# Performance work log

Measured on AMD Instinct MI355X. Metric: run time of the kernel, lower is better.

The kernel has to match this reference:

```python
import jax, jax.numpy as jnp
import numpy as np

NH = 1024
VS = 50257
CUT0 = 1675          # round(VS/30)
CUT1 = 3 * CUT0      # 5025
N_CLUSTERS = 2
HEAD_SIZE = CUT0 + N_CLUSTERS          # 1677
D0, D1 = NH // 4, NH // 16             # 256, 64
SZ0, SZ1 = CUT1 - CUT0, VS - CUT1      # 3350, 45232


def setup_inputs() -> dict:
    key = jax.random.key(0)
    ks = jax.random.split(key, 8)
    s = 0.02
    return {
        "x": jax.random.normal(ks[0], (8, 512, NH), dtype=jnp.float32),
        "y": jax.random.randint(ks[1], (8, 512), 0, VS, dtype=jnp.int64),
        "head_w": jax.random.normal(ks[2], (HEAD_SIZE, NH), dtype=jnp.float32) * s,
        "head_b": jnp.zeros((HEAD_SIZE,), dtype=jnp.float32),
        "proj0": jax.random.normal(ks[3], (D0, NH), dtype=jnp.float32) * s,
        "w0": jax.random.normal(ks[4], (SZ0, D0), dtype=jnp.float32) * s,
        "proj1": jax.random.normal(ks[5], (D1, NH), dtype=jnp.float32) * s,
        "w1": jax.random.normal(ks[6], (SZ1, D1), dtype=jnp.float32) * s,
    }


def reference(x, y, head_w, head_b, proj0, w0, proj1, w1):
    # Flatten as in the torch forward: x -> [N, nh], y -> [N]
    xf = x.reshape(-1, x.shape[-1])            # [N, NH]
    yf = y.reshape(-1)                         # [N]

    # Head: shortlist tokens + 2 cluster logits
    head_logits = jnp.einsum('nh,vh->nv', xf, head_w) + head_b   # [N, 1677]
    head_lp = jax.nn.log_softmax(head_logits, axis=-1)

    # Default: target in head shortlist
    in_head = yf < CUT0
    idx_head = jnp.where(in_head, yf, 0)
    out = jnp.take_along_axis(head_lp, idx_head[:, None], axis=1)[:, 0]

    # Tail clusters: dense per-cluster small GEMMs + log-softmax, masked select
    for i, (low, high, proj, w) in enumerate(
            [(CUT0, CUT1, proj0, w0), (CUT1, VS, proj1, w1)]):
        size = high - low
        h = jnp.einsum('nh,dh->nd', xf, proj)          # [N, d_i]
        lp = jax.nn.log_softmax(jnp.einsum('nd,vd->nv', h, w), axis=-1)  # [N, size]
        rel = jnp.clip(yf - low, 0, size - 1)
        cl = head_lp[:, CUT0 + i] + jnp.take_along_axis(lp, rel[:, None], axis=1)[:, 0]
        mask = (yf >= low) & (yf < high)
        out = jnp.where(mask, cl, out)

    loss = -jnp.mean(out)
    return out, loss
```

## Files before the change

kernel.cpp:

```cpp
#include <hip/hip_runtime.h>
#include <stdint.h>

#define NROWS 4096
#define NHID 1024
#define CC0 1675
#define CC1 5025
#define HEADSZ 1677
#define PD0 256
#define PD1 64
#define TSZ0 3350
#define TSZ1 45232
#define HPN (HEADSZ + PD0 + PD1)
#define TPC1 6
#define L2E 1.4426950408889634f
#define LN2 0.6931471805599453f

#define NB_HD 896
#define NB_PJ 192
#define NB_CW 512
#define NB_MID (NB_HD + NB_PJ + NB_CW)

#define NB_C1 1888
#define NB_C0 864
#define NB_TG 1024
#define NB_TAIL (NB_C1 + NB_C0 + NB_TG)

typedef __attribute__((ext_vector_type(8))) __bf16 bf16x8;
typedef __attribute__((ext_vector_type(4))) float f32x4;

__device__ __forceinline__ unsigned short f2bf(float f) {
  union { float f; uint32_t u; } v; v.f = f;
  return (unsigned short)((v.u + 0x7FFFu + ((v.u >> 16) & 1u)) >> 16);
}
__device__ __forceinline__ float bfl(uint32_t u) {
  union { uint32_t u; float f; } v; v.u = u << 16; return v.f;
}
__device__ __forceinline__ float bfh(uint32_t u) {
  union { uint32_t u; float f; } v; v.u = u & 0xFFFF0000u; return v.f;
}
__device__ __forceinline__ float bf1(unsigned short u) {
  union { uint32_t u; float f; } v; v.u = ((uint32_t)u) << 16; return v.f;
}
#define EXP2(x) __builtin_amdgcn_exp2f(x)

#define CV1 1048576
#define CV2 1477888
#define CV3 1543424
#define CV4 1559808
#define CV5 1774208
#define CV6 2497920
#define CVW0 (CV5 - CV4)
#define CVW  (CV6 - CV4)

__global__ void conv_part(const float* __restrict__ x, const float* __restrict__ hw,
                          const float* __restrict__ p0, const float* __restrict__ p1,
                          unsigned short* __restrict__ dst,
                          const int* __restrict__ y,
                          int* __restrict__ idx0, int* __restrict__ pos0,
                          int* __restrict__ idx1, int* __restrict__ pos1,
                          int* __restrict__ n01,
                          float* __restrict__ hs3, float* __restrict__ outp) {
  if (blockIdx.x >= 1025) {
    int z = blockIdx.x - 1025;
    for (int i = z * 256 + (int)threadIdx.x; i < 3 * NROWS; i += 7 * 256)
      hs3[i] = 0.f;
    if (z == 0 && threadIdx.x == 0) outp[NROWS] = 0.f;
    return;
  }
  if (blockIdx.x == 1024) {
    __shared__ int sc0[256], sc1[256], nsh[2];
    int t = threadIdx.x;
    int yl[16];
    int c0 = 0, c1 = 0;
#pragma unroll
    for (int k = 0; k < 16; ++k) {
      int yv = y[t * 16 + k];
      yl[k] = yv;
      c0 += (yv >= CC0 && yv < CC1);
      c1 += (yv >= CC1);
    }
    sc0[t] = c0; sc1[t] = c1;
    __syncthreads();
    if (t == 0) {
      int a0 = 0, a1 = 0;
      for (int i = 0; i < 256; ++i) {
        int v0 = sc0[i]; sc0[i] = a0; a0 += v0;
        int v1 = sc1[i]; sc1[i] = a1; a1 += v1;
      }
      n01[0] = a0; n01[1] = a1; nsh[0] = a0; nsh[1] = a1;
    }
    __syncthreads();
    int p0c = sc0[t], p1c = sc1[t];
#pragma unroll
    for (int k = 0; k < 16; ++k) {
      int n = t * 16 + k, yv = yl[k];
      if (yv >= CC0 && yv < CC1) { idx0[p0c] = n; pos0[n] = p0c; ++p0c; }
      else if (yv >= CC1)        { idx1[p1c] = n; pos1[n] = p1c; ++p1c; }
    }
    for (int j = nsh[0] + t; j < NROWS; j += 256) idx0[j] = 0;
    for (int j = nsh[1] + t; j < NROWS; j += 256) idx1[j] = 0;
    return;
  }
  const int stride = 1024 * 256;
  for (int i = blockIdx.x * 256 + threadIdx.x; i < CV4; i += stride) {
    const float* src; int off; float sc;
    if (i < CV1)      { src = x;  off = i;       sc = 1.f; }
    else if (i < CV2) { src = hw; off = i - CV1; sc = L2E; }
    else if (i < CV3) { src = p0; off = i - CV2; sc = 1.f; }
    else              { src = p1; off = i - CV3; sc = 1.f; }
    float4 v = reinterpret_cast<const float4*>(src)[off];
    ushort4 o;
    o.x = f2bf(v.x * sc); o.y = f2bf(v.y * sc);
    o.z = f2bf(v.z * sc); o.w = f2bf(v.w * sc);
    reinterpret_cast<ushort4*>(dst)[i] = o;
  }
}

#define GLOAD(g, l) __builtin_amdgcn_global_load_lds( \
    (const __attribute__((address_space(1))) uint32_t*)(const void*)(g), \
    (__attribute__((address_space(3))) uint32_t*)(void*)(l), 16, 0, 0)

#define SWZB(L) ((L) ^ ((((L) >> 7) & 7) << 4))

__device__ __forceinline__
void gemm_core(const unsigned short* __restrict__ A, int lda,
               const unsigned short* __restrict__ B, int ldb,
               int N, int K, int tile0, int tile1, int brow,
               const float* __restrict__ bias,
               float* __restrict__ sum_out,
               unsigned short* __restrict__ Cout, int ldc, int coutStart,
               unsigned short* AsB, unsigned short* BsB,
               const int* __restrict__ gidx) {
  const int tid = threadIdx.x;
  const int lane = tid & 63;
  const int wid = tid >> 6;
  const int wrow = (wid >> 1) * 64;
  const int wcol = (wid & 1) * 64;
  const int lr = lane & 15, lg = lane >> 4;
  const int nsteps = (tile1 - tile0) * (K >> 5);
  const int rowBase = brow + wrow;

  int arowc[2];
#pragma unroll
  for (int c = 0; c < 2; ++c) {
    int g = wid * 128 + c * 64 + lane;
    int S = SWZB(g * 16);
    int row = S >> 6;
    arowc[c] = gidx ? gidx[brow + row] : brow + row;
  }

  float sacc[4][4];
#pragma unroll
  for (int m = 0; m < 4; ++m)
#pragma unroll
    for (int r = 0; r < 4; ++r) sacc[m][r] = 0.f;

  auto stage = [&](int b, int tt, int kk) {
#pragma unroll
    for (int c = 0; c < 2; ++c) {
      int g = wid * 128 + c * 64 + lane;
      int L = g * 16;
      int S = SWZB(L);
      int row = S >> 6, ko = (S >> 4) & 3;
      GLOAD(A + (size_t)arowc[c] * lda + kk + ko * 8, (char*)AsB + b * 8192 + L);
      int bsrc = tt * 128 + row; bsrc = bsrc < N ? bsrc : N - 1;
      GLOAD(B + (size_t)bsrc * ldb + kk + ko * 8, (char*)BsB + b * 8192 + L);
    }
  };

  f32x4 acc[4][4];
#pragma unroll
  for (int m = 0; m < 4; ++m)
#pragma unroll
    for (int n = 0; n < 4; ++n) acc[m][n] = (f32x4){0.f, 0.f, 0.f, 0.f};

  int tp = tile0, kp = 0;
  auto adv = [&](int& t, int& k) { k += 32; if (k == K) { k = 0; ++t; } };
  stage(0, tp, kp); adv(tp, kp);
  if (nsteps > 1) { stage(1, tp, kp); adv(tp, kp); }

  int tile = tile0, k0 = 0;
  for (int s = 0; s < nsteps; ++s) {
    if (s + 1 < nsteps) asm volatile("s_waitcnt vmcnt(4)" ::: "memory");
    else                asm volatile("s_waitcnt vmcnt(0)" ::: "memory");
    __builtin_amdgcn_s_barrier();
    if (s + 2 < nsteps) { stage((s + 2) % 3, tp, kp); adv(tp, kp); }

    const int cur = s % 3;
    int k0n = k0 + 32, tn = tile;
    if (k0n == K) { k0n = 0; tn = tile + 1; }

    bf16x8 af[4], bfv[4];
#pragma unroll
    for (int m = 0; m < 4; ++m)
      af[m] = *(const bf16x8*)((const char*)AsB + cur * 8192 +
                               SWZB((wrow + m * 16 + lr) * 64 + lg * 16));
#pragma unroll
    for (int n = 0; n < 4; ++n)
      bfv[n] = *(const bf16x8*)((const char*)BsB + cur * 8192 +
                                SWZB((wcol + n * 16 + lr) * 64 + lg * 16));
#pragma unroll
    for (int m = 0; m < 4; ++m)
#pragma unroll
      for (int n = 0; n < 4; ++n)
        acc[m][n] = __builtin_amdgcn_mfma_f32_16x16x32_bf16(af[m], bfv[n], acc[m][n], 0, 0, 0);

    if (tn != tile) {
      const int cb = tile * 128 + wcol;
#pragma unroll
      for (int m = 0; m < 4; ++m)
#pragma unroll
        for (int n = 0; n < 4; ++n) {
#pragma unroll
          for (int r = 0; r < 4; ++r) {
            int col = cb + n * 16 + lr;
            if (col < N) {
              float v = acc[m][n][r];
              if (Cout && col >= coutStart) {
                int row = rowBase + m * 16 + lg * 4 + r;
                Cout[(size_t)row * ldc + (col - coutStart)] = f2bf(v);
              } else {
                if (bias) v = fmaf(bias[col], L2E, v);
                sacc[m][r] += EXP2(v);
              }
            }
          }
          acc[m][n] = (f32x4){0.f, 0.f, 0.f, 0.f};
        }
    }
    tile = tn; k0 = k0n;
  }

#pragma unroll
  for (int m = 0; m < 4; ++m)
#pragma unroll
    for (int r = 0; r < 4; ++r) {
      float s = sacc[m][r];
      s += __shfl_xor(s, 1); s += __shfl_xor(s, 2);
      s += __shfl_xor(s, 4); s += __shfl_xor(s, 8);
      if (lr == 0) atomicAdd(&sum_out[rowBase + m * 16 + lg * 4 + r], s);
    }
}

__device__ __forceinline__
void gemm_core3(const unsigned short* __restrict__ A, int lda,
                const unsigned short* __restrict__ B, int ldb,
                int N, int K, int tile0, int brow,
                const float* __restrict__ bias,
                float* __restrict__ sum_out,
                unsigned short* __restrict__ Cout, int ldc,
                char* AsB, char* BsB) {
  const int tid = threadIdx.x;
  const int lane = tid & 63;
  const int wid = tid >> 6;
  const int wrow = (wid >> 1) * 32;
  const int wcol = (wid & 1) * 64;
  const int lr = lane & 15, lg = lane >> 4;
  const int nsteps = K >> 6;
  const int rowBase = brow + wrow;

  auto stage = [&](int b, int kk) {
#pragma unroll
    for (int kh = 0; kh < 2; ++kh) {
      {
        int L4 = tid * 16;
        int S = SWZB(L4);
        int row = S >> 6, ko = (S >> 4) & 3;
        GLOAD(A + (size_t)(brow + row) * lda + kk + kh * 32 + ko * 8,
              AsB + b * 8192 + kh * 4096 + L4);
      }
#pragma unroll
      for (int c = 0; c < 2; ++c) {
        int L8 = (c * 256 + tid) * 16;
        int S = SWZB(L8);
        int col = S >> 6, ko = (S >> 4) & 3;
        int bsrc = tile0 * 128 + col; bsrc = bsrc < N ? bsrc : N - 1;
        GLOAD(B + (size_t)bsrc * ldb + kk + kh * 32 + ko * 8,
              BsB + b * 16384 + kh * 8192 + L8);
      }
    }
  };

  f32x4 acc[2][4];
#pragma unroll
  for (int m = 0; m < 2; ++m)
#pragma unroll
    for (int n = 0; n < 4; ++n) acc[m][n] = (f32x4){0.f, 0.f, 0.f, 0.f};

  stage(0, 0);
  asm volatile("s_waitcnt vmcnt(0)" ::: "memory");
  __builtin_amdgcn_s_barrier();

  for (int s = 0; s < nsteps; ++s) {
    if (s + 1 < nsteps) stage((s + 1) & 1, (s + 1) * 64);
    const int cur = s & 1;
#pragma unroll
    for (int kh = 0; kh < 2; ++kh) {
      bf16x8 af[2], bfv[4];
#pragma unroll
      for (int m = 0; m < 2; ++m)
        af[m] = *(const bf16x8*)(AsB + cur * 8192 + kh * 4096 +
                                 SWZB((wrow + m * 16 + lr) * 64 + lg * 16));
#pragma unroll
      for (int n = 0; n < 4; ++n)
        bfv[n] = *(const bf16x8*)(BsB + cur * 16384 + kh * 8192 +
                                  SWZB((wcol + n * 16 + lr) * 64 + lg * 16));
#pragma unroll
      for (int m = 0; m < 2; ++m)
#pragma unroll
        for (int n = 0; n < 4; ++n)
          acc[m][n] = __builtin_amdgcn_mfma_f32_16x16x32_bf16(af[m], bfv[n], acc[m][n], 0, 0, 0);
    }
    if (s + 1 < nsteps) {
      asm volatile("s_waitcnt vmcnt(0)" ::: "memory");
      __builtin_amdgcn_s_barrier();
    }
  }

  const int cb = tile0 * 128 + wcol;
  float sacc[2][4];
#pragma unroll
  for (int m = 0; m < 2; ++m)
#pragma unroll
    for (int r = 0; r < 4; ++r) sacc[m][r] = 0.f;
#pragma unroll
  for (int m = 0; m < 2; ++m)
#pragma unroll
    for (int n = 0; n < 4; ++n)
#pragma unroll
      for (int r = 0; r < 4; ++r) {
        int col = cb + n * 16 + lr;
        if (col < N) {
          float v = acc[m][n][r];
          if (Cout) {
            int row = rowBase + m * 16 + lg * 4 + r;
            Cout[(size_t)row * ldc + col] = f2bf(v);
          } else {
            if (bias) v = fmaf(bias[col], L2E, v);
            sacc[m][r] += EXP2(v);
          }
        }
      }
  if (sum_out) {
#pragma unroll
    for (int m = 0; m < 2; ++m)
#pragma unroll
      for (int r = 0; r < 4; ++r) {
        float s = sacc[m][r];
        s += __shfl_xor(s, 1); s += __shfl_xor(s, 2);
        s += __shfl_xor(s, 4); s += __shfl_xor(s, 8);
        if (lr == 0) atomicAdd(&sum_out[rowBase + m * 16 + lg * 4 + r], s);
      }
  }
}

__global__ __launch_bounds__(256, 3)
void fused_mid(const unsigned short* __restrict__ xb,
               const unsigned short* __restrict__ hpb,
               const float* __restrict__ head_b,
               float* __restrict__ hs,
               unsigned short* __restrict__ hb,
               const float* __restrict__ w0f, const float* __restrict__ w1f,
               unsigned short* __restrict__ dstAll) {
  __shared__ __align__(16) char lds[49152];
  const int bid = blockIdx.x;

  if (bid < NB_HD) {
    const int xcd = bid & 7;
    const int local = bid >> 3;
    const int rowBlk = xcd * 8 + local / 14;
    const int colChunk = local % 14;
    gemm_core3(xb, NHID, hpb, NHID, HEADSZ, NHID, colChunk, rowBlk * 64,
               head_b, hs, nullptr, 0, lds, lds + 16384);
    return;
  }

  if (bid < NB_HD + NB_PJ) {
    const int b1 = bid - NB_HD;
    const int cpx = NB_PJ >> 3;
    const int sid = (b1 & 7) * cpx + (b1 >> 3);
    const int rowBlk = sid & 63;
    const int colChunk = sid >> 6;
    gemm_core3(xb, NHID, hpb + (size_t)HEADSZ * NHID, NHID, PD0 + PD1, NHID,
               colChunk, rowBlk * 64,
               nullptr, nullptr, hb, PD0 + PD1, lds, lds + 16384);
    return;
  }

  {
    const int b2 = bid - NB_HD - NB_PJ;
    const int stride = NB_CW * 256;
    for (int i = b2 * 256 + (int)threadIdx.x; i < CVW; i += stride) {
      const float* src; int off;
      if (i < CVW0) { src = w0f; off = i; }
      else          { src = w1f; off = i - CVW0; }
      float4 v = reinterpret_cast<const float4*>(src)[off];
      ushort4 o;
      o.x = f2bf(v.x * L2E); o.y = f2bf(v.y * L2E);
      o.z = f2bf(v.z * L2E); o.w = f2bf(v.w * L2E);
      reinterpret_cast<ushort4*>(dstAll)[CV4 + i] = o;
    }
  }
}

__global__ __launch_bounds__(256, 3)
void fused_tail(const unsigned short* __restrict__ hb,
                const unsigned short* __restrict__ w0b,
                const unsigned short* __restrict__ w1b,
                const unsigned short* __restrict__ xb,
                const unsigned short* __restrict__ hwb,
                const float* __restrict__ head_b,
                const int* __restrict__ y,
                const int* __restrict__ idx0, const int* __restrict__ idx1,
                const int* __restrict__ n01,
                float* __restrict__ s0, float* __restrict__ s1,
                float* __restrict__ ht, float* __restrict__ tc) {
  __shared__ __align__(16) unsigned short lds[6 * 4096];
  const int bid = blockIdx.x;

  if (bid < NB_C1) {
    const int tid = threadIdx.x;
    const int lane = tid & 63;
    const int wid = tid >> 6;
    const int lr = lane & 15, lg = lane >> 4;
    const int cpx = NB_C1 >> 3;
    const int sid = (bid & 7) * cpx + (bid >> 3);
    const int rowBlk = sid & 31;
    const int colChunk = sid >> 5;
    if (rowBlk * 128 >= n01[1]) return;
    const int rowBase = rowBlk * 128 + (wid >> 1) * 64;
    const int wcol = (wid & 1) * 64;
    const int tile0 = colChunk * TPC1;

    int colOff[4], srcOff[4];
#pragma unroll
    for (int c = 0; c < 4; ++c) {
      int L = (c * 256 + tid) * 16;
      int S = L ^ (((L >> 7) & 7) << 4);
      colOff[c] = S >> 7;
      srcOff[c] = (S & 127) >> 1;
    }
    auto stage = [&](int b, int t) {
#pragma unroll
      for (int c = 0; c < 4; ++c) {
        int gc = t * 128 + colOff[c];
        gc = gc < TSZ1 ? gc : TSZ1 - 1;
        GLOAD(w1b + (size_t)gc * PD1 + srcOff[c],
              (char*)lds + b * 16384 + (c * 256 + tid) * 16);
      }
    };

    bf16x8 af[4][2];
#pragma unroll
    for (int m = 0; m < 4; ++m) {
      int ridx = idx1[rowBase + m * 16 + lr];
      const unsigned short* p = hb + PD0 +
          (size_t)ridx * (PD0 + PD1) + lg * 8;
      af[m][0] = *(const bf16x8*)p;
      af[m][1] = *(const bf16x8*)(p + 32);
    }

    float sacc[4][4];
#pragma unroll
    for (int m = 0; m < 4; ++m)
#pragma unroll
      for (int r = 0; r < 4; ++r) sacc[m][r] = 0.f;

    stage(0, tile0);
    stage(1, tile0 + 1);

#pragma unroll 1
    for (int s = 0; s < TPC1; ++s) {
      if (s + 1 < TPC1) asm volatile("s_waitcnt vmcnt(4)" ::: "memory");
      else              asm volatile("s_waitcnt vmcnt(0)" ::: "memory");
      __builtin_amdgcn_s_barrier();
      if (s + 2 < TPC1) stage((s + 2) % 3, tile0 + s + 2);

      const int cur = s % 3;
      const int cb = (tile0 + s) * 128 + wcol;
      const int full = (cb + 63 < TSZ1);

#pragma unroll
      for (int nh = 0; nh < 2; ++nh) {
        bf16x8 bf[2][2];
#pragma unroll
        for (int nn = 0; nn < 2; ++nn) {
          int ccol = wcol + (nh * 2 + nn) * 16 + lr;
#pragma unroll
          for (int kh = 0; kh < 2; ++kh) {
            int L = ccol * 128 + kh * 64 + lg * 16;
            bf[nn][kh] = *(const bf16x8*)((const char*)lds + cur * 16384 +
                                          (L ^ ((ccol & 7) << 4)));
          }
        }
        f32x4 acc[4][2];
#pragma unroll
        for (int m = 0; m < 4; ++m)
#pragma unroll
          for (int nn = 0; nn < 2; ++nn) {
            f32x4 a = (f32x4){0.f, 0.f, 0.f, 0.f};
            a = __builtin_amdgcn_mfma_f32_16x16x32_bf16(af[m][0], bf[nn][0], a, 0, 0, 0);
            a = __builtin_amdgcn_mfma_f32_16x16x32_bf16(af[m][1], bf[nn][1], a, 0, 0, 0);
            acc[m][nn] = a;
          }
        if (full) {
#pragma unroll
          for (int m = 0; m < 4; ++m)
#pragma unroll
            for (int r = 0; r < 4; ++r)
              sacc[m][r] += EXP2(acc[m][0][r]) + EXP2(acc[m][1][r]);
        } else {
#pragma unroll
          for (int m = 0; m < 4; ++m)
#pragma unroll
            for (int r = 0; r < 4; ++r) {
              float t = 0.f;
#pragma unroll
              for (int nn = 0; nn < 2; ++nn)
                if (cb + (nh * 2 + nn) * 16 + lr < TSZ1) t += EXP2(acc[m][nn][r]);
              sacc[m][r] += t;
            }
        }
      }
    }

#pragma unroll
    for (int m = 0; m < 4; ++m)
#pragma unroll
      for (int r = 0; r < 4; ++r) {
        float s = sacc[m][r];
        s += __shfl_xor(s, 1); s += __shfl_xor(s, 2);
        s += __shfl_xor(s, 4); s += __shfl_xor(s, 8);
        if (lr == 0) atomicAdd(&s1[rowBase + m * 16 + lg * 4 + r], s);
      }
    return;
  }

  if (bid < NB_C1 + NB_C0) {
    const int b0 = bid - NB_C1;
    const int cpx = NB_C0 >> 3;
    const int sid = (b0 & 7) * cpx + (b0 >> 3);
    const int rowBlk = sid & 31;
    const int colChunk = sid >> 5;
    if (rowBlk * 128 >= n01[0]) return;
    gemm_core(hb, PD0 + PD1, w0b, PD0, TSZ0, PD0, colChunk, colChunk + 1,
              rowBlk * 128, nullptr, s0, nullptr, 0, 0,
              (unsigned short*)lds, (unsigned short*)lds + 3 * 4096, idx0);
    return;
  }

  {
    const int b2 = bid - NB_C1 - NB_C0;
    int row = b2 * 4 + (threadIdx.x >> 6);
    int lane = threadIdx.x & 63;
    int yv = y[row];
    int th = yv < CC0 ? yv : (yv < CC1 ? CC0 : CC0 + 1);

    const unsigned short* xr = xb + (size_t)row * NHID + lane * 16;
    const unsigned short* wr = hwb + (size_t)th * NHID + lane * 16;
    uint4 xa = *(const uint4*)xr,       wa = *(const uint4*)wr;
    uint4 xc = *(const uint4*)(xr + 8), wc = *(const uint4*)(wr + 8);
    float s = 0.f;
    uint32_t xs[8] = {xa.x, xa.y, xa.z, xa.w, xc.x, xc.y, xc.z, xc.w};
    uint32_t ws[8] = {wa.x, wa.y, wa.z, wa.w, wc.x, wc.y, wc.z, wc.w};
#pragma unroll
    for (int j = 0; j < 8; ++j)
      s += bfl(xs[j]) * bfl(ws[j]) + bfh(xs[j]) * bfh(ws[j]);
#pragma unroll
    for (int d = 1; d < 64; d <<= 1) s += __shfl_xor(s, d);

    float cl = 0.f;
    if (yv >= CC0) {
      if (yv < CC1) {
        int rel = yv - CC0;
        const unsigned short* hr = hb + (size_t)row * (PD0 + PD1) + lane * 4;
        const unsigned short* w0r = w0b + (size_t)rel * PD0 + lane * 4;
        uint2 ha = *(const uint2*)hr, wa0 = *(const uint2*)w0r;
        cl = bfl(ha.x) * bfl(wa0.x) + bfh(ha.x) * bfh(wa0.x)
           + bfl(ha.y) * bfl(wa0.y) + bfh(ha.y) * bfh(wa0.y);
      } else {
        int rel = yv - CC1;
        cl = bf1(hb[(size_t)row * (PD0 + PD1) + PD0 + lane])
           * bf1(w1b[(size_t)rel * PD1 + lane]);
      }
#pragma unroll
      for (int d = 1; d < 64; d <<= 1) cl += __shfl_xor(cl, d);
    }
    if (lane == 0) { ht[row] = s * LN2 + head_b[th]; tc[row] = (yv < CC0) ? 0.f : cl; }
  }
}

__global__ void rowloss(const float* __restrict__ hs, const float* __restrict__ ht,
                        const float* __restrict__ s0, const float* __restrict__ s1,
                        const float* __restrict__ tc,
                        const int* __restrict__ pos0, const int* __restrict__ pos1,
                        const int* __restrict__ y, float* __restrict__ out) {
  int n = blockIdx.x * 256 + threadIdx.x;
  int yv = y[n];
  float o = ht[n] - __builtin_amdgcn_logf(hs[n]) * LN2;
  if (yv >= CC0) {
    float sv = (yv < CC1) ? s0[pos0[n]] : s1[pos1[n]];
    o += tc[n] * LN2 - __builtin_amdgcn_logf(sv) * LN2;
  }
  out[n] = o;
  float l = o;
#pragma unroll
  for (int d = 1; d < 64; d <<= 1) l += __shfl_xor(l, d);
  __shared__ float red[4];
  if ((threadIdx.x & 63) == 0) red[threadIdx.x >> 6] = l;
  __syncthreads();
  if (threadIdx.x == 0)
    atomicAdd(&out[NROWS], -(red[0] + red[1] + red[2] + red[3]) / (float)NROWS);
}

extern "C" void kernel_launch(void* const* d_in, const int* in_sizes, int n_in,
                              void* d_out, int out_size, void* d_ws, size_t ws_size,
                              hipStream_t stream) {
  const float* x      = (const float*)d_in[0];
  const int*   y      = (const int*)d_in[1];
  const float* head_w = (const float*)d_in[2];
  const float* head_b = (const float*)d_in[3];
  const float* proj0  = (const float*)d_in[4];
  const float* w0     = (const float*)d_in[5];
  const float* proj1  = (const float*)d_in[6];
  const float* w1     = (const float*)d_in[7];
  float* out = (float*)d_out;

  char* wp = (char*)d_ws;
  unsigned short* xb  = (unsigned short*)wp; wp += (size_t)NROWS * NHID * 2;
  unsigned short* hpb = (unsigned short*)wp; wp += (size_t)HPN * NHID * 2;
  unsigned short* w0b = (unsigned short*)wp; wp += (size_t)TSZ0 * PD0 * 2;
  unsigned short* w1b = (unsigned short*)wp; wp += (size_t)TSZ1 * PD1 * 2;
  unsigned short* hb  = (unsigned short*)wp; wp += (size_t)NROWS * (PD0 + PD1) * 2;
  float* hs = (float*)wp; wp += NROWS * 4;
  float* s0 = (float*)wp; wp += NROWS * 4;
  float* s1 = (float*)wp; wp += NROWS * 4;
  float* ht = (float*)wp; wp += NROWS * 4;
  float* tc = (float*)wp; wp += NROWS * 4;
  int* idx0 = (int*)wp; wp += NROWS * 4;
  int* pos0 = (int*)wp; wp += NROWS * 4;
  int* idx1 = (int*)wp; wp += NROWS * 4;
  int* pos1 = (int*)wp; wp += NROWS * 4;
  int* n01  = (int*)wp; wp += 8 * 4;

  conv_part<<<dim3(1032), 256, 0, stream>>>(
      x, head_w, proj0, proj1, xb, y, idx0, pos0, idx1, pos1, n01, hs, out);

  fused_mid<<<dim3(NB_MID), 256, 0, stream>>>(
      xb, hpb, head_b, hs, hb, w0, w1, xb);

  fused_tail<<<dim3(NB_TAIL), 256, 0, stream>>>(
      hb, w0b, w1b, xb, hpb, head_b, y, idx0, idx1, n01, s0, s1, ht, tc);

  rowloss<<<dim3(NROWS / 256), 256, 0, stream>>>(
      hs, ht, s0, s1, tc, pos0, pos1, y, out);
}
```

Measured before the change: 97.79 us.

## Switch head/projection GEMM to triple-buffered K=32 pipeline with partial waits

After: 96.70 us. Within noise of the previous version (-1.1%).

```diff
diff --git a/kernel.cpp b/kernel.cpp
--- a/kernel.cpp
+++ b/kernel.cpp
@@ -243,7 +243,7 @@
 }
 
 __device__ __forceinline__
-void gemm_core3(const unsigned short* __restrict__ A, int lda,
+void gemm_core4(const unsigned short* __restrict__ A, int lda,
                 const unsigned short* __restrict__ B, int ldb,
                 int N, int K, int tile0, int brow,
                 const float* __restrict__ bias,
@@ -256,29 +256,29 @@
   const int wrow = (wid >> 1) * 32;
   const int wcol = (wid & 1) * 64;
   const int lr = lane & 15, lg = lane >> 4;
-  const int nsteps = K >> 6;
+  const int nsteps = K >> 5;
   const int rowBase = brow + wrow;
 
+  const int aL = tid * 16;
+  const int aS = SWZB(aL);
+  const int arow = aS >> 6, ako = ((aS >> 4) & 3) * 8;
+  int bcol[2], bko[2];
+#pragma unroll
+  for (int c = 0; c < 2; ++c) {
+    int L = (c * 256 + tid) * 16;
+    int S = SWZB(L);
+    int col = S >> 6;
+    int bsrc = tile0 * 128 + col;
+    bcol[c] = bsrc < N ? bsrc : N - 1;
+    bko[c] = ((S >> 4) & 3) * 8;
+  }
+
   auto stage = [&](int b, int kk) {
-#pragma unroll
-    for (int kh = 0; kh < 2; ++kh) {
-      {
-        int L4 = tid * 16;
-        int S = SWZB(L4);
-        int row = S >> 6, ko = (S >> 4) & 3;
-        GLOAD(A + (size_t)(brow + row) * lda + kk + kh * 32 + ko * 8,
-              AsB + b * 8192 + kh * 4096 + L4);
-      }
-#pragma unroll
-      for (int c = 0; c < 2; ++c) {
-        int L8 = (c * 256 + tid) * 16;
-        int S = SWZB(L8);
-        int col = S >> 6, ko = (S >> 4) & 3;
-        int bsrc = tile0 * 128 + col; bsrc = bsrc < N ? bsrc : N - 1;
-        GLOAD(B + (size_t)bsrc * ldb + kk + kh * 32 + ko * 8,
-              BsB + b * 16384 + kh * 8192 + L8);
-      }
-    }
+    GLOAD(A + (size_t)(brow + arow) * lda + kk + ako, AsB + b * 4096 + aL);
+#pragma unroll
+    for (int c = 0; c < 2; ++c)
+      GLOAD(B + (size_t)bcol[c] * ldb + kk + bko[c],
+            BsB + b * 8192 + (c * 256 + tid) * 16);
   };
 
   f32x4 acc[2][4];
@@ -288,33 +288,29 @@
     for (int n = 0; n < 4; ++n) acc[m][n] = (f32x4){0.f, 0.f, 0.f, 0.f};
 
   stage(0, 0);
-  asm volatile("s_waitcnt vmcnt(0)" ::: "memory");
-  __builtin_amdgcn_s_barrier();
+  stage(1, 32);
 
   for (int s = 0; s < nsteps; ++s) {
-    if (s + 1 < nsteps) stage((s + 1) & 1, (s + 1) * 64);
-    const int cur = s & 1;
-#pragma unroll
-    for (int kh = 0; kh < 2; ++kh) {
-      bf16x8 af[2], bfv[4];
-#pragma unroll
-      for (int m = 0; m < 2; ++m)
-        af[m] = *(const bf16x8*)(AsB + cur * 8192 + kh * 4096 +
-                                 SWZB((wrow + m * 16 + lr) * 64 + lg * 16));
+    if (s + 1 < nsteps) asm volatile("s_waitcnt vmcnt(3)" ::: "memory");
+    else                asm volatile("s_waitcnt vmcnt(0)" ::: "memory");
+    __builtin_amdgcn_s_barrier();
+    if (s + 2 < nsteps) stage((s + 2) % 3, (s + 2) * 32);
+
+    const int cur = s % 3;
+    bf16x8 af[2], bfv[4];
+#pragma unroll
+    for (int m = 0; m < 2; ++m)
+      af[m] = *(const bf16x8*)(AsB + cur * 4096 +
+                               SWZB((wrow + m * 16 + lr) * 64 + lg * 16));
+#pragma unroll
+    for (int n = 0; n < 4; ++n)
+      bfv[n] = *(const bf16x8*)(BsB + cur * 8192 +
+                                SWZB((wcol + n * 16 + lr) * 64 + lg * 16));
+#pragma unroll
+    for (int m = 0; m < 2; ++m)
 #pragma unroll
       for (int n = 0; n < 4; ++n)
-        bfv[n] = *(const bf16x8*)(BsB + cur * 16384 + kh * 8192 +
-                                  SWZB((wcol + n * 16 + lr) * 64 + lg * 16));
-#pragma unroll
-      for (int m = 0; m < 2; ++m)
-#pragma unroll
-        for (int n = 0; n < 4; ++n)
-          acc[m][n] = __builtin_amdgcn_mfma_f32_16x16x32_bf16(af[m], bfv[n], acc[m][n], 0, 0, 0);
-    }
-    if (s + 1 < nsteps) {
-      asm volatile("s_waitcnt vmcnt(0)" ::: "memory");
-      __builtin_amdgcn_s_barrier();
-    }
+        acc[m][n] = __builtin_amdgcn_mfma_f32_16x16x32_bf16(af[m], bfv[n], acc[m][n], 0, 0, 0);
   }
 
   const int cb = tile0 * 128 + wcol;
@@ -354,7 +350,7 @@
   }
 }
 
-__global__ __launch_bounds__(256, 3)
+__global__ __launch_bounds__(256, 4)
 void fused_mid(const unsigned short* __restrict__ xb,
                const unsigned short* __restrict__ hpb,
                const float* __restrict__ head_b,
@@ -362,7 +358,7 @@
                unsigned short* __restrict__ hb,
                const float* __restrict__ w0f, const float* __restrict__ w1f,
                unsigned short* __restrict__ dstAll) {
-  __shared__ __align__(16) char lds[49152];
+  __shared__ __align__(16) char lds[36864];
   const int bid = blockIdx.x;
 
   if (bid < NB_HD) {
@@ -370,8 +366,8 @@
     const int local = bid >> 3;
     const int rowBlk = xcd * 8 + local / 14;
     const int colChunk = local % 14;
-    gemm_core3(xb, NHID, hpb, NHID, HEADSZ, NHID, colChunk, rowBlk * 64,
-               head_b, hs, nullptr, 0, lds, lds + 16384);
+    gemm_core4(xb, NHID, hpb, NHID, HEADSZ, NHID, colChunk, rowBlk * 64,
+               head_b, hs, nullptr, 0, lds, lds + 12288);
     return;
   }
 
@@ -381,9 +377,9 @@
     const int sid = (b1 & 7) * cpx + (b1 >> 3);
     const int rowBlk = sid & 63;
     const int colChunk = sid >> 6;
-    gemm_core3(xb, NHID, hpb + (size_t)HEADSZ * NHID, NHID, PD0 + PD1, NHID,
+    gemm_core4(xb, NHID, hpb + (size_t)HEADSZ * NHID, NHID, PD0 + PD1, NHID,
                colChunk, rowBlk * 64,
-               nullptr, nullptr, hb, PD0 + PD1, lds, lds + 16384);
+               nullptr, nullptr, hb, PD0 + PD1, lds, lds + 12288);
     return;
   }
 
```
